# Kernel optimization log

Hardware: AMD Instinct MI355X
Metric: run time of the kernel (lower is better)

Reference implementation:

```python
import jax, jax.numpy as jnp
import numpy as np

VOCAB = 50257
D_MODEL = 768
N_LAYERS = 4
N_HEADS = 12
D_HEAD = D_MODEL // N_HEADS
MAX_LEN = 5000
EPS = 1e-5


def _make_pe(max_len, d_model):
    # sinusoidal PE, interleaved sin/cos, base n=10000 (matches PositionalEncodingLayer)
    pos = jnp.arange(max_len, dtype=jnp.float32)[:, None]            # [L,1]
    i = jnp.arange(d_model // 2, dtype=jnp.float32)[None, :]         # [1,D/2]
    theta = pos / jnp.power(10000.0, 2.0 * i / d_model)              # [L,D/2]
    pe = jnp.zeros((max_len, d_model), dtype=jnp.float32)
    pe = pe.at[:, 0::2].set(jnp.sin(theta))
    pe = pe.at[:, 1::2].set(jnp.cos(theta))
    return pe


def setup_inputs() -> dict:
    key = jax.random.key(0)
    ks = jax.random.split(key, 10)
    B, S = 2, 1024
    tokens = jax.random.randint(ks[0], (B, S), 0, VOCAB)
    std = 0.02
    embed = jax.random.normal(ks[1], (VOCAB, D_MODEL), jnp.float32) * std
    pe = _make_pe(MAX_LEN, D_MODEL)
    # per-layer stacked params, torch nn.Linear convention: y = x @ W.T + b
    wq_w = jax.random.normal(ks[2], (N_LAYERS, D_MODEL, D_MODEL), jnp.float32) * std
    wk_w = jax.random.normal(ks[3], (N_LAYERS, D_MODEL, D_MODEL), jnp.float32) * std
    wv_w = jax.random.normal(ks[4], (N_LAYERS, D_MODEL, D_MODEL), jnp.float32) * std
    lin_w = jax.random.normal(ks[5], (N_LAYERS, D_MODEL, D_MODEL), jnp.float32) * std
    wq_b = jnp.zeros((N_LAYERS, D_MODEL), jnp.float32)
    wk_b = jnp.zeros((N_LAYERS, D_MODEL), jnp.float32)
    wv_b = jnp.zeros((N_LAYERS, D_MODEL), jnp.float32)
    lin_b = jnp.zeros((N_LAYERS, D_MODEL), jnp.float32)
    n1_s = jnp.ones((N_LAYERS, D_MODEL), jnp.float32)
    n1_b = jnp.zeros((N_LAYERS, D_MODEL), jnp.float32)
    n2_s = jnp.ones((N_LAYERS, D_MODEL), jnp.float32)
    n2_b = jnp.zeros((N_LAYERS, D_MODEL), jnp.float32)
    unembed_w = jax.random.normal(ks[6], (VOCAB, D_MODEL), jnp.float32) * std
    unembed_b = jnp.zeros((VOCAB,), jnp.float32)
    return dict(tokens=tokens, embed=embed, pe=pe,
                wq_w=wq_w, wq_b=wq_b, wk_w=wk_w, wk_b=wk_b, wv_w=wv_w, wv_b=wv_b,
                lin_w=lin_w, lin_b=lin_b, n1_s=n1_s, n1_b=n1_b, n2_s=n2_s, n2_b=n2_b,
                unembed_w=unembed_w, unembed_b=unembed_b)


def _layernorm(x, scale, bias):
    m = jnp.mean(x, axis=-1, keepdims=True)
    v = jnp.mean(jnp.square(x - m), axis=-1, keepdims=True)
    return (x - m) * jax.lax.rsqrt(v + EPS) * scale + bias


def _attn_block(x, wq_w, wq_b, wk_w, wk_b, wv_w, wv_b, lin_w, lin_b, n1_s, n1_b, n2_s, n2_b):
    B, S, D = x.shape
    def proj(w, b):
        y = x @ w.T + b
        return y.reshape(B, S, N_HEADS, D_HEAD).transpose(0, 2, 1, 3)  # [B,H,S,Dh]
    q, k, v = proj(wq_w, wq_b), proj(wk_w, wk_b), proj(wv_w, wv_b)
    scores = jnp.einsum('bhqd,bhkd->bhqk', q, k) / jnp.sqrt(jnp.float32(D_HEAD))
    causal = jnp.tril(jnp.ones((S, S), dtype=bool))
    scores = jnp.where(causal, scores, -jnp.inf)
    probs = jax.nn.softmax(scores, axis=-1)
    attn = jnp.einsum('bhqk,bhkd->bhqd', probs, v)
    attn = attn.transpose(0, 2, 1, 3).reshape(B, S, D)
    x = _layernorm(x + attn, n1_s, n1_b)
    x = _layernorm(x + (x @ lin_w.T + lin_b), n2_s, n2_b)
    return x


def reference(tokens, embed, pe, wq_w, wq_b, wk_w, wk_b, wv_w, wv_b,
              lin_w, lin_b, n1_s, n1_b, n2_s, n2_b, unembed_w, unembed_b):
    B, S = tokens.shape
    x = embed[tokens] + pe[:S]
    for l in range(N_LAYERS):
        x = _attn_block(x, wq_w[l], wq_b[l], wk_w[l], wk_b[l], wv_w[l], wv_b[l],
                        lin_w[l], lin_b[l], n1_s[l], n1_b[l], n2_s[l], n2_b[l])
    logits = x @ unembed_w.T + unembed_b
    return logits
```

## Files before the change

kernel.cpp:

```cpp
#include <hip/hip_runtime.h>
#include <hip/hip_bf16.h>


#define VOCAB 50257
#define DM 768
#define NL 4
#define NH 12
#define DH 64
#define SEQ 1024
#define BATCH 2
#define ROWS (BATCH * SEQ)
#define QKVN (3 * DM)

typedef __attribute__((ext_vector_type(8))) short short8;
typedef __attribute__((ext_vector_type(4))) float f32x4;

__device__ __forceinline__ unsigned short f2bf(float f) {
    union { float f; unsigned u; } v; v.f = f;
    unsigned r = v.u + 0x7FFFu + ((v.u >> 16) & 1u);
    return (unsigned short)(r >> 16);
}

#define GLOAD16(gp, lp)                                                        \
    __builtin_amdgcn_global_load_lds(                                          \
        (const __attribute__((address_space(1))) unsigned int*)(gp),           \
        (__attribute__((address_space(3))) unsigned int*)(lp), 16, 0, 0)

#define BARRIER() asm volatile("s_barrier" ::: "memory")
#define VMCNT0()  asm volatile("s_waitcnt vmcnt(0)" ::: "memory")

__global__ __launch_bounds__(256) void cvt_kernel(const float* __restrict__ in,
                                                  unsigned short* __restrict__ out,
                                                  int n4) {
    int i = blockIdx.x * 256 + threadIdx.x;
    if (i < n4) {
        float4 v = ((const float4*)in)[i];
        ushort4 o;
        o.x = f2bf(v.x); o.y = f2bf(v.y); o.z = f2bf(v.z); o.w = f2bf(v.w);
        ((ushort4*)out)[i] = o;
    }
}

__global__ __launch_bounds__(256) void cvt_qkv_kernel(const float* __restrict__ wq,
                                                      const float* __restrict__ wk,
                                                      const float* __restrict__ wv,
                                                      unsigned short* __restrict__ dst,
                                                      int n4) {
    int i = blockIdx.x * 256 + threadIdx.x;
    if (i >= n4) return;
    const int PER_L = 3 * DM * DM / 4, PER_W = DM * DM / 4;
    int l = i / PER_L;
    int rem = i - l * PER_L;
    int w = rem / PER_W;
    int r2 = rem - w * PER_W;
    const float* src = (w == 0) ? wq : (w == 1) ? wk : wv;
    float4 v = ((const float4*)src)[(size_t)l * PER_W + r2];
    ushort4 o;
    o.x = f2bf(v.x); o.y = f2bf(v.y); o.z = f2bf(v.z); o.w = f2bf(v.w);
    ((ushort4*)dst)[i] = o;
}

__global__ __launch_bounds__(256) void pack_qkv_bias(const float* __restrict__ bq,
                                                     const float* __restrict__ bk,
                                                     const float* __restrict__ bv,
                                                     float* __restrict__ dst) {
    int i = blockIdx.x * 256 + threadIdx.x;
    if (i >= NL * QKVN) return;
    int l = i / QKVN, c = i - l * QKVN;
    int w = c / DM, cc = c - w * DM;
    const float* src = (w == 0) ? bq : (w == 1) ? bk : bv;
    dst[i] = src[l * DM + cc];
}

__global__ __launch_bounds__(256) void embed_kernel(const int* __restrict__ tok,
                                                    const float* __restrict__ emb,
                                                    const float* __restrict__ pe,
                                                    float* __restrict__ xf,
                                                    unsigned short* __restrict__ xb) {
    int row = blockIdx.x;
    int t = tok[row];
    int s = row & (SEQ - 1);
    #pragma unroll
    for (int j = 0; j < 3; ++j) {
        int c = threadIdx.x + j * 256;
        float v = emb[(size_t)t * DM + c] + pe[(size_t)s * DM + c];
        xf[(size_t)row * DM + c] = v;
        xb[(size_t)row * DM + c] = f2bf(v);
    }
}

__device__ __forceinline__ float block_sum(float x, float* red) {
    #pragma unroll
    for (int off = 32; off > 0; off >>= 1) x += __shfl_down(x, off);
    int w = threadIdx.x >> 6;
    if ((threadIdx.x & 63) == 0) red[w] = x;
    __syncthreads();
    float t = (red[0] + red[1]) + (red[2] + red[3]);
    __syncthreads();
    return t;
}

__global__ __launch_bounds__(256) void ln_kernel(const float* __restrict__ A,
                                                 const float* __restrict__ Bi,
                                                 const float* __restrict__ sc,
                                                 const float* __restrict__ bi,
                                                 float* __restrict__ xf,
                                                 unsigned short* __restrict__ xb) {
    __shared__ float red[4];
    int row = blockIdx.x, tid = threadIdx.x;
    const float* ap = A + (size_t)row * DM;
    const float* bp = Bi + (size_t)row * DM;
    float v[3], sum = 0.f;
    #pragma unroll
    for (int j = 0; j < 3; ++j) { v[j] = ap[tid + j * 256] + bp[tid + j * 256]; sum += v[j]; }
    sum = block_sum(sum, red);
    float mean = sum * (1.f / DM);
    float vs = 0.f;
    #pragma unroll
    for (int j = 0; j < 3; ++j) { float d = v[j] - mean; vs += d * d; }
    vs = block_sum(vs, red);
    float rstd = rsqrtf(vs * (1.f / DM) + 1e-5f);
    #pragma unroll
    for (int j = 0; j < 3; ++j) {
        int c = tid + j * 256;
        float o = (v[j] - mean) * rstd * sc[c] + bi[c];
        xf[(size_t)row * DM + c] = o;
        xb[(size_t)row * DM + c] = f2bf(o);
    }
}

template <int OUT_BF16>
__global__ __launch_bounds__(256, 2) void gemm128db(const unsigned short* __restrict__ A,
                                                    const unsigned short* __restrict__ B,
                                                    const float* __restrict__ bias,
                                                    void* __restrict__ C,
                                                    int M, int N, int K, int gx) {
    __shared__ __align__(16) unsigned short As[2][128 * 64];
    __shared__ __align__(16) unsigned short Bs[2][128 * 64];
    int bid = blockIdx.x;
    const int nwg = gridDim.x;
    if ((nwg & 7) == 0) {
        int q = nwg >> 3;
        bid = (bid & 7) * q + (bid >> 3);
    }
    const int bx = bid % gx, by = bid / gx;
    const int m0 = bx * 128, n0 = by * 128;
    const int tid = threadIdx.x, lane = tid & 63, wid = tid >> 6;
    const int wm = wid >> 1, wn = wid & 1;
    const int lr = lane & 15, lq = lane >> 4;

    const int sr = wid * 32 + (lane >> 3);
    const int sch = lane & 7;
    const int scs = sch ^ (sr & 7);
    const unsigned short* aP[4];
    const unsigned short* bP[4];
    int sO[4];
    #pragma unroll
    for (int i = 0; i < 4; ++i) {
        int r = sr + i * 8;
        aP[i] = A + (size_t)(m0 + r) * K + scs * 8;
        int br = n0 + r; if (br >= N) br = N - 1;
        bP[i] = B + (size_t)br * K + scs * 8;
        sO[i] = r * 64 + sch * 8;
    }

#define STG(t, c)                                                              \
    do { _Pragma("unroll")                                                     \
        for (int _i = 0; _i < 4; ++_i)                                         \
            GLOAD16(aP[_i] + (t) * 64, &As[c][sO[_i]]);                        \
        _Pragma("unroll")                                                      \
        for (int _i = 0; _i < 4; ++_i)                                         \
            GLOAD16(bP[_i] + (t) * 64, &Bs[c][sO[_i]]);                        \
    } while (0)

    f32x4 acc[4][4] = {};
    const int NT = K >> 6;

    STG(0, 0);
    VMCNT0();
    BARRIER();

    int cur = 0;
    for (int t = 0; t < NT; ++t) {
        if (t + 1 < NT) STG(t + 1, cur ^ 1);
        #pragma unroll
        for (int kk = 0; kk < 2; ++kk) {
            short8 a[4], b[4];
            #pragma unroll
            for (int i = 0; i < 4; ++i) {
                int ar = wm * 64 + i * 16 + lr;
                a[i] = *reinterpret_cast<const short8*>(
                    &As[cur][ar * 64 + (((kk * 4 + lq) ^ (ar & 7)) * 8)]);
                int br = wn * 64 + i * 16 + lr;
                b[i] = *reinterpret_cast<const short8*>(
                    &Bs[cur][br * 64 + (((kk * 4 + lq) ^ (br & 7)) * 8)]);
            }
            __builtin_amdgcn_s_setprio(1);
            #pragma unroll
            for (int i = 0; i < 4; ++i)
                #pragma unroll
                for (int j = 0; j < 4; ++j)
                    acc[i][j] = __builtin_amdgcn_mfma_f32_16x16x32_bf16(a[i], b[j], acc[i][j], 0, 0, 0);
            __builtin_amdgcn_s_setprio(0);
        }
        VMCNT0();
        BARRIER();
        cur ^= 1;
    }

    #pragma unroll
    for (int i = 0; i < 4; ++i) {
        int row = m0 + wm * 64 + i * 16 + lq * 4;
        #pragma unroll
        for (int j = 0; j < 4; ++j) {
            int col = n0 + wn * 64 + j * 16 + lr;
            if (col < N) {
                float bv = bias[col];
                #pragma unroll
                for (int r = 0; r < 4; ++r) {
                    float v = acc[i][j][r] + bv;
                    if (OUT_BF16) ((unsigned short*)C)[(size_t)(row + r) * N + col] = f2bf(v);
                    else          ((float*)C)[(size_t)(row + r) * N + col] = v;
                }
            }
        }
    }
#undef STG
}

__global__ __launch_bounds__(256) void attn_kernel(const unsigned short* __restrict__ Q,
                                                   const unsigned short* __restrict__ K,
                                                   const unsigned short* __restrict__ V,
                                                   int ld,
                                                   float* __restrict__ O) {
    __shared__ __align__(16) unsigned short Ks[64 * 64];
    __shared__ __align__(16) unsigned short Vs[64 * 64];
    __shared__ __align__(16) unsigned short Ps[4][16 * 64];
    const int qb = blockIdx.x;
    const int bh = blockIdx.y;
    const int b = bh / NH, h = bh % NH;
    const int tid = threadIdx.x, lane = tid & 63, w = tid >> 6;
    const int lr = lane & 15, lq = lane >> 4;
    const int wq0 = qb * 64 + w * 16;
    const size_t base = (size_t)b * SEQ * ld + h * DH;
    const size_t obase = (size_t)b * SEQ * DM + h * DH;

    short8 qf[2];
    {
        const unsigned short* qp = Q + base + (size_t)(wq0 + lr) * ld + lq * 8;
        qf[0] = *reinterpret_cast<const short8*>(qp);
        qf[1] = *reinterpret_cast<const short8*>(qp + 32);
    }
    f32x4 o_acc[4] = {};
    float mrow[4], lrow[4];
    #pragma unroll
    for (int r = 0; r < 4; ++r) { mrow[r] = -1e30f; lrow[r] = 0.f; }

    const int srow = tid >> 3, scol = (tid & 7) * 8;
    for (int t = 0; t <= qb; ++t) {
        const int kv0 = t * 64;
        #pragma unroll
        for (int rr = 0; rr < 2; ++rr) {
            int row = rr * 32 + srow;
            {
                const unsigned short* kp = K + base + (size_t)(kv0 + row) * ld + scol;
                short8 v = *reinterpret_cast<const short8*>(kp);
                *reinterpret_cast<short8*>(&Ks[(row * 64 + scol) ^ ((row & 7) << 3)]) = v;
            }
            {
                const unsigned short* vp = V + base + (size_t)(kv0 + row) * ld + scol;
                short8 v = *reinterpret_cast<const short8*>(vp);
                #pragma unroll
                for (int j = 0; j < 8; ++j) {
                    int d = scol + j;
                    Vs[(d * 64 + row) ^ ((d & 7) << 3)] = (unsigned short)v[j];
                }
            }
        }
        __syncthreads();
        if (kv0 <= wq0 + 15) {
            f32x4 s[4];
            #pragma unroll
            for (int n = 0; n < 4; ++n) {
                int br = n * 16 + lr;
                short8 b0 = *reinterpret_cast<const short8*>(&Ks[(br * 64 + lq * 8) ^ ((br & 7) << 3)]);
                short8 b1 = *reinterpret_cast<const short8*>(&Ks[(br * 64 + 32 + lq * 8) ^ ((br & 7) << 3)]);
                f32x4 z = {};
                z = __builtin_amdgcn_mfma_f32_16x16x32_bf16(qf[0], b0, z, 0, 0, 0);
                z = __builtin_amdgcn_mfma_f32_16x16x32_bf16(qf[1], b1, z, 0, 0, 0);
                s[n] = z;
            }
            const bool diag = (t == qb);
            #pragma unroll
            for (int n = 0; n < 4; ++n)
                #pragma unroll
                for (int r = 0; r < 4; ++r) {
                    float v = s[n][r] * 0.125f;
                    if (diag) {
                        int rg = wq0 + lq * 4 + r;
                        int cg = kv0 + n * 16 + lr;
                        if (cg > rg) v = -1e30f;
                    }
                    s[n][r] = v;
                }
            float f[4];
            #pragma unroll
            for (int r = 0; r < 4; ++r) {
                float mx = fmaxf(fmaxf(s[0][r], s[1][r]), fmaxf(s[2][r], s[3][r]));
                #pragma unroll
                for (int off = 1; off < 16; off <<= 1) mx = fmaxf(mx, __shfl_xor(mx, off));
                float mn = fmaxf(mrow[r], mx);
                f[r] = exp2f((mrow[r] - mn) * 1.44269504f);
                mrow[r] = mn;
            }
            #pragma unroll
            for (int n = 0; n < 4; ++n)
                #pragma unroll
                for (int r = 0; r < 4; ++r)
                    s[n][r] = exp2f((s[n][r] - mrow[r]) * 1.44269504f);
            #pragma unroll
            for (int r = 0; r < 4; ++r) {
                float ls = ((s[0][r] + s[1][r]) + (s[2][r] + s[3][r]));
                #pragma unroll
                for (int off = 1; off < 16; off <<= 1) ls += __shfl_xor(ls, off);
                lrow[r] = lrow[r] * f[r] + ls;
            }
            #pragma unroll
            for (int n = 0; n < 4; ++n)
                #pragma unroll
                for (int r = 0; r < 4; ++r) {
                    int pr = lq * 4 + r, pc = n * 16 + lr;
                    Ps[w][(pr * 64 + pc) ^ ((pr & 7) << 3)] = f2bf(s[n][r]);
                }
            #pragma unroll
            for (int n = 0; n < 4; ++n)
                #pragma unroll
                for (int r = 0; r < 4; ++r) o_acc[n][r] *= f[r];
            #pragma unroll
            for (int kk = 0; kk < 2; ++kk) {
                short8 pa = *reinterpret_cast<const short8*>(
                    &Ps[w][(lr * 64 + kk * 32 + lq * 8) ^ ((lr & 7) << 3)]);
                #pragma unroll
                for (int n = 0; n < 4; ++n) {
                    int vr = n * 16 + lr;
                    short8 bv = *reinterpret_cast<const short8*>(
                        &Vs[(vr * 64 + kk * 32 + lq * 8) ^ ((vr & 7) << 3)]);
                    o_acc[n] = __builtin_amdgcn_mfma_f32_16x16x32_bf16(pa, bv, o_acc[n], 0, 0, 0);
                }
            }
        }
        __syncthreads();
    }
    #pragma unroll
    for (int r = 0; r < 4; ++r) {
        float inv = 1.f / lrow[r];
        int row = wq0 + lq * 4 + r;
        #pragma unroll
        for (int n = 0; n < 4; ++n)
            O[obase + (size_t)row * DM + n * 16 + lr] = o_acc[n][r] * inv;
    }
}

extern "C" void kernel_launch(void* const* d_in, const int* in_sizes, int n_in,
                              void* d_out, int out_size, void* d_ws, size_t ws_size,
                              hipStream_t stream) {
    const int*   tokens   = (const int*)d_in[0];
    const float* embed    = (const float*)d_in[1];
    const float* pe       = (const float*)d_in[2];
    const float* wq_w     = (const float*)d_in[3];
    const float* wq_b     = (const float*)d_in[4];
    const float* wk_w     = (const float*)d_in[5];
    const float* wk_b     = (const float*)d_in[6];
    const float* wv_w     = (const float*)d_in[7];
    const float* wv_b     = (const float*)d_in[8];
    const float* lin_w    = (const float*)d_in[9];
    const float* lin_b    = (const float*)d_in[10];
    const float* n1_s     = (const float*)d_in[11];
    const float* n1_b     = (const float*)d_in[12];
    const float* n2_s     = (const float*)d_in[13];
    const float* n2_b     = (const float*)d_in[14];
    const float* unemb_w  = (const float*)d_in[15];
    const float* unemb_b  = (const float*)d_in[16];

    char* ws = (char*)d_ws;
    size_t off = 0;
    auto carve = [&](size_t bytes) { char* p = ws + off; off += (bytes + 255) & ~(size_t)255; return p; };
    float*          xf     = (float*)carve((size_t)ROWS * DM * 4);
    float*          yb     = (float*)carve((size_t)ROWS * DM * 4);
    unsigned short* xb     = (unsigned short*)carve((size_t)ROWS * DM * 2);
    unsigned short* qkv    = (unsigned short*)carve((size_t)ROWS * QKVN * 2);
    unsigned short* wqkv_h = (unsigned short*)carve((size_t)NL * QKVN * DM * 2);
    unsigned short* lin_h  = (unsigned short*)carve((size_t)NL * DM * DM * 2);
    unsigned short* ue_h   = (unsigned short*)carve((size_t)VOCAB * DM * 2);
    float*          qkvb   = (float*)carve((size_t)NL * QKVN * 4);

    {
        int nq4 = NL * QKVN * DM / 4;
        cvt_qkv_kernel<<<(nq4 + 255) / 256, 256, 0, stream>>>(wq_w, wk_w, wv_w, wqkv_h, nq4);
        int nl4 = NL * DM * DM / 4;
        cvt_kernel<<<(nl4 + 255) / 256, 256, 0, stream>>>(lin_w, lin_h, nl4);
        int nu4 = VOCAB * DM / 4;
        cvt_kernel<<<(nu4 + 255) / 256, 256, 0, stream>>>(unemb_w, ue_h, nu4);
        pack_qkv_bias<<<(NL * QKVN + 255) / 256, 256, 0, stream>>>(wq_b, wk_b, wv_b, qkvb);
    }
    embed_kernel<<<ROWS, 256, 0, stream>>>(tokens, embed, pe, xf, xb);

    const int gx = ROWS / 128;
    for (int l = 0; l < NL; ++l) {
        gemm128db<1><<<gx * (QKVN / 128), 256, 0, stream>>>(
            xb, wqkv_h + (size_t)l * QKVN * DM, qkvb + l * QKVN, qkv,
            ROWS, QKVN, DM, gx);
        attn_kernel<<<dim3(SEQ / 64, BATCH * NH), 256, 0, stream>>>(
            qkv, qkv + DM, qkv + 2 * DM, QKVN, yb);
        ln_kernel<<<ROWS, 256, 0, stream>>>(xf, yb, n1_s + l * DM, n1_b + l * DM, xf, xb);
        gemm128db<0><<<gx * (DM / 128), 256, 0, stream>>>(
            xb, lin_h + (size_t)l * DM * DM, lin_b + l * DM, yb,
            ROWS, DM, DM, gx);
        ln_kernel<<<ROWS, 256, 0, stream>>>(xf, yb, n2_s + l * DM, n2_b + l * DM, xf, xb);
    }
    const int gyu = (VOCAB + 127) / 128;
    gemm128db<0><<<gx * gyu, 256, 0, stream>>>(
        xb, ue_h, unemb_b, (float*)d_out, ROWS, VOCAB, DM, gx);
}
```

Before: 865.6 us.

## Shrink GEMM tiles to 64x64 and use one wavefront per row in layernorm

Replaces the 128x128 double-buffered GEMM with a 64x64 tile variant that launches more blocks with higher occupancy, and drops the MFMA priority hints. The layernorm kernel now gives each row to a single wavefront, using float4 loads and shuffle-only reductions with no shared memory or block barriers. Smaller tiles raise parallelism for the small-N projection GEMMs but lower arithmetic intensity and reuse, which may hurt the large vocabulary GEMM that dominates runtime.

Result: slower. 921.6 us (+6.5%).

```diff
diff --git a/kernel.cpp b/kernel.cpp
--- a/kernel.cpp
+++ b/kernel.cpp
@@ -89,54 +89,64 @@
     }
 }
 
-__device__ __forceinline__ float block_sum(float x, float* red) {
-    #pragma unroll
-    for (int off = 32; off > 0; off >>= 1) x += __shfl_down(x, off);
-    int w = threadIdx.x >> 6;
-    if ((threadIdx.x & 63) == 0) red[w] = x;
-    __syncthreads();
-    float t = (red[0] + red[1]) + (red[2] + red[3]);
-    __syncthreads();
-    return t;
-}
-
 __global__ __launch_bounds__(256) void ln_kernel(const float* __restrict__ A,
                                                  const float* __restrict__ Bi,
                                                  const float* __restrict__ sc,
                                                  const float* __restrict__ bi,
                                                  float* __restrict__ xf,
                                                  unsigned short* __restrict__ xb) {
-    __shared__ float red[4];
-    int row = blockIdx.x, tid = threadIdx.x;
+    const int w = threadIdx.x >> 6, lane = threadIdx.x & 63;
+    const int row = blockIdx.x * 4 + w;
     const float* ap = A + (size_t)row * DM;
     const float* bp = Bi + (size_t)row * DM;
-    float v[3], sum = 0.f;
-    #pragma unroll
-    for (int j = 0; j < 3; ++j) { v[j] = ap[tid + j * 256] + bp[tid + j * 256]; sum += v[j]; }
-    sum = block_sum(sum, red);
+    float4 v[3];
+    float sum = 0.f;
+    #pragma unroll
+    for (int j = 0; j < 3; ++j) {
+        int c4 = lane * 3 + j;
+        float4 a4 = ((const float4*)ap)[c4];
+        float4 b4 = ((const float4*)bp)[c4];
+        v[j].x = a4.x + b4.x; v[j].y = a4.y + b4.y;
+        v[j].z = a4.z + b4.z; v[j].w = a4.w + b4.w;
+        sum += (v[j].x + v[j].y) + (v[j].z + v[j].w);
+    }
+    #pragma unroll
+    for (int off = 32; off > 0; off >>= 1) sum += __shfl_xor(sum, off);
     float mean = sum * (1.f / DM);
     float vs = 0.f;
     #pragma unroll
-    for (int j = 0; j < 3; ++j) { float d = v[j] - mean; vs += d * d; }
-    vs = block_sum(vs, red);
+    for (int j = 0; j < 3; ++j) {
+        float dx = v[j].x - mean, dy = v[j].y - mean, dz = v[j].z - mean, dw = v[j].w - mean;
+        vs += dx * dx + dy * dy + dz * dz + dw * dw;
+    }
+    #pragma unroll
+    for (int off = 32; off > 0; off >>= 1) vs += __shfl_xor(vs, off);
     float rstd = rsqrtf(vs * (1.f / DM) + 1e-5f);
     #pragma unroll
     for (int j = 0; j < 3; ++j) {
-        int c = tid + j * 256;
-        float o = (v[j] - mean) * rstd * sc[c] + bi[c];
-        xf[(size_t)row * DM + c] = o;
-        xb[(size_t)row * DM + c] = f2bf(o);
+        int c4 = lane * 3 + j;
+        float4 s4 = ((const float4*)sc)[c4];
+        float4 b4 = ((const float4*)bi)[c4];
+        float4 o;
+        o.x = (v[j].x - mean) * rstd * s4.x + b4.x;
+        o.y = (v[j].y - mean) * rstd * s4.y + b4.y;
+        o.z = (v[j].z - mean) * rstd * s4.z + b4.z;
+        o.w = (v[j].w - mean) * rstd * s4.w + b4.w;
+        ((float4*)(xf + (size_t)row * DM))[c4] = o;
+        ushort4 h;
+        h.x = f2bf(o.x); h.y = f2bf(o.y); h.z = f2bf(o.z); h.w = f2bf(o.w);
+        ((ushort4*)(xb + (size_t)row * DM))[c4] = h;
     }
 }
 
 template <int OUT_BF16>
-__global__ __launch_bounds__(256, 2) void gemm128db(const unsigned short* __restrict__ A,
-                                                    const unsigned short* __restrict__ B,
-                                                    const float* __restrict__ bias,
-                                                    void* __restrict__ C,
-                                                    int M, int N, int K, int gx) {
-    __shared__ __align__(16) unsigned short As[2][128 * 64];
-    __shared__ __align__(16) unsigned short Bs[2][128 * 64];
+__global__ __launch_bounds__(256, 5) void gemm64h(const unsigned short* __restrict__ A,
+                                                  const unsigned short* __restrict__ B,
+                                                  const float* __restrict__ bias,
+                                                  void* __restrict__ C,
+                                                  int M, int N, int K, int gx) {
+    __shared__ __align__(16) unsigned short As[2][64 * 64];
+    __shared__ __align__(16) unsigned short Bs[2][64 * 64];
     int bid = blockIdx.x;
     const int nwg = gridDim.x;
     if ((nwg & 7) == 0) {
@@ -144,20 +154,20 @@
         bid = (bid & 7) * q + (bid >> 3);
     }
     const int bx = bid % gx, by = bid / gx;
-    const int m0 = bx * 128, n0 = by * 128;
+    const int m0 = bx * 64, n0 = by * 64;
     const int tid = threadIdx.x, lane = tid & 63, wid = tid >> 6;
     const int wm = wid >> 1, wn = wid & 1;
     const int lr = lane & 15, lq = lane >> 4;
 
-    const int sr = wid * 32 + (lane >> 3);
-    const int sch = lane & 7;
+    const int sr = tid >> 3;
+    const int sch = tid & 7;
     const int scs = sch ^ (sr & 7);
-    const unsigned short* aP[4];
-    const unsigned short* bP[4];
-    int sO[4];
-    #pragma unroll
-    for (int i = 0; i < 4; ++i) {
-        int r = sr + i * 8;
+    const unsigned short* aP[2];
+    const unsigned short* bP[2];
+    int sO[2];
+    #pragma unroll
+    for (int i = 0; i < 2; ++i) {
+        int r = sr + i * 32;
         aP[i] = A + (size_t)(m0 + r) * K + scs * 8;
         int br = n0 + r; if (br >= N) br = N - 1;
         bP[i] = B + (size_t)br * K + scs * 8;
@@ -166,14 +176,14 @@
 
 #define STG(t, c)                                                              \
     do { _Pragma("unroll")                                                     \
-        for (int _i = 0; _i < 4; ++_i)                                         \
+        for (int _i = 0; _i < 2; ++_i)                                         \
             GLOAD16(aP[_i] + (t) * 64, &As[c][sO[_i]]);                        \
         _Pragma("unroll")                                                      \
-        for (int _i = 0; _i < 4; ++_i)                                         \
+        for (int _i = 0; _i < 2; ++_i)                                         \
             GLOAD16(bP[_i] + (t) * 64, &Bs[c][sO[_i]]);                        \
     } while (0)
 
-    f32x4 acc[4][4] = {};
+    f32x4 acc[2][2] = {};
     const int NT = K >> 6;
 
     STG(0, 0);
@@ -185,23 +195,21 @@
         if (t + 1 < NT) STG(t + 1, cur ^ 1);
         #pragma unroll
         for (int kk = 0; kk < 2; ++kk) {
-            short8 a[4], b[4];
-            #pragma unroll
-            for (int i = 0; i < 4; ++i) {
-                int ar = wm * 64 + i * 16 + lr;
+            short8 a[2], b[2];
+            #pragma unroll
+            for (int i = 0; i < 2; ++i) {
+                int ar = wm * 32 + i * 16 + lr;
                 a[i] = *reinterpret_cast<const short8*>(
                     &As[cur][ar * 64 + (((kk * 4 + lq) ^ (ar & 7)) * 8)]);
-                int br = wn * 64 + i * 16 + lr;
+                int br = wn * 32 + i * 16 + lr;
                 b[i] = *reinterpret_cast<const short8*>(
                     &Bs[cur][br * 64 + (((kk * 4 + lq) ^ (br & 7)) * 8)]);
             }
-            __builtin_amdgcn_s_setprio(1);
-            #pragma unroll
-            for (int i = 0; i < 4; ++i)
-                #pragma unroll
-                for (int j = 0; j < 4; ++j)
+            #pragma unroll
+            for (int i = 0; i < 2; ++i)
+                #pragma unroll
+                for (int j = 0; j < 2; ++j)
                     acc[i][j] = __builtin_amdgcn_mfma_f32_16x16x32_bf16(a[i], b[j], acc[i][j], 0, 0, 0);
-            __builtin_amdgcn_s_setprio(0);
         }
         VMCNT0();
         BARRIER();
@@ -209,11 +217,11 @@
     }
 
     #pragma unroll
-    for (int i = 0; i < 4; ++i) {
-        int row = m0 + wm * 64 + i * 16 + lq * 4;
+    for (int i = 0; i < 2; ++i) {
+        int row = m0 + wm * 32 + i * 16 + lq * 4;
         #pragma unroll
-        for (int j = 0; j < 4; ++j) {
-            int col = n0 + wn * 64 + j * 16 + lr;
+        for (int j = 0; j < 2; ++j) {
+            int col = n0 + wn * 32 + j * 16 + lr;
             if (col < N) {
                 float bv = bias[col];
                 #pragma unroll
@@ -405,20 +413,20 @@
     }
     embed_kernel<<<ROWS, 256, 0, stream>>>(tokens, embed, pe, xf, xb);
 
-    const int gx = ROWS / 128;
+    const int gx = ROWS / 64;
     for (int l = 0; l < NL; ++l) {
-        gemm128db<1><<<gx * (QKVN / 128), 256, 0, stream>>>(
+        gemm64h<1><<<gx * (QKVN / 64), 256, 0, stream>>>(
             xb, wqkv_h + (size_t)l * QKVN * DM, qkvb + l * QKVN, qkv,
             ROWS, QKVN, DM, gx);
         attn_kernel<<<dim3(SEQ / 64, BATCH * NH), 256, 0, stream>>>(
             qkv, qkv + DM, qkv + 2 * DM, QKVN, yb);
-        ln_kernel<<<ROWS, 256, 0, stream>>>(xf, yb, n1_s + l * DM, n1_b + l * DM, xf, xb);
-        gemm128db<0><<<gx * (DM / 128), 256, 0, stream>>>(
+        ln_kernel<<<ROWS / 4, 256, 0, stream>>>(xf, yb, n1_s + l * DM, n1_b + l * DM, xf, xb);
+        gemm64h<0><<<gx * (DM / 64), 256, 0, stream>>>(
             xb, lin_h + (size_t)l * DM * DM, lin_b + l * DM, yb,
             ROWS, DM, DM, gx);
-        ln_kernel<<<ROWS, 256, 0, stream>>>(xf, yb, n2_s + l * DM, n2_b + l * DM, xf, xb);
-    }
-    const int gyu = (VOCAB + 127) / 128;
-    gemm128db<0><<<gx * gyu, 256, 0, stream>>>(
+        ln_kernel<<<ROWS / 4, 256, 0, stream>>>(xf, yb, n2_s + l * DM, n2_b + l * DM, xf, xb);
+    }
+    const int gyu = (VOCAB + 63) / 64;
+    gemm64h<0><<<gx * gyu, 256, 0, stream>>>(
         xb, ue_h, unemb_b, (float*)d_out, ROWS, VOCAB, DM, gx);
 }
```
